# Optimization experiments

Hardware: AMD Instinct MI355X
Metric: run time of the kernel (lower is better)

Reference implementation:

```python
import jax, jax.numpy as jnp
import numpy as np

K_NBR = 64  # max_num_neighbors in radius()
M1, M2, M3 = 2048, 512, 512  # fps sample counts: 4096*0.5, 2048*0.25, 512*1.0
R1, R2, R3 = 0.2, 0.4, 1.0


def _fps_idx(pos, m):
    # Furthest point sampling, deterministic start at index 0. pos: [N,3] -> idx [m]
    d2 = jnp.sum((pos - pos[0]) ** 2, axis=-1)  # [N]

    def step(min_d2, _):
        nxt = jnp.argmax(min_d2).astype(jnp.int32)
        min_d2 = jnp.minimum(min_d2, jnp.sum((pos - pos[nxt]) ** 2, axis=-1))
        return min_d2, nxt

    _, rest = jax.lax.scan(step, d2, None, length=m - 1)
    return jnp.concatenate([jnp.zeros((1,), jnp.int32), rest])


def _ball_query(pos_src, pos_q, r, k):
    # Nearest up-to-k neighbors within radius r. Returns idx [M,k], valid mask [M,k].
    d2 = (jnp.sum(pos_q ** 2, -1)[:, None] + jnp.sum(pos_src ** 2, -1)[None, :]
          - 2.0 * pos_q @ pos_src.T)  # [M,N]
    neg = jnp.where(d2 <= r * r, -d2, -jnp.inf)
    vals, idx = jax.lax.top_k(neg, k)
    return idx, vals > -jnp.inf


def _sa_layer(x, pos, m, r, w1, b1, w2, b2):
    # x: [B,N,C], pos: [B,N,3] -> (x_new [B,m,Cout], pos_new [B,m,3])
    idx = jax.vmap(lambda p: _fps_idx(p, m))(pos)                     # [B,m]
    pos_q = jnp.take_along_axis(pos, idx[..., None], axis=1)         # [B,m,3]
    nbr, mask = jax.vmap(lambda s, q: _ball_query(s, q, r, K_NBR))(pos, pos_q)
    gather = jax.vmap(lambda a, i: a[i])                              # [N,C],[m,k]->[m,k,C]
    x_j = gather(x, nbr)                                              # [B,m,k,C]
    pos_j = gather(pos, nbr)                                          # [B,m,k,3]
    # PointNetConv message: MLP(concat(x_j, pos_j - pos_i)), max-aggregate
    msg = jnp.concatenate([x_j, pos_j - pos_q[:, :, None, :]], axis=-1)
    h = jnp.maximum(msg @ w1 + b1, 0.0) @ w2 + b2                     # [B,m,k,Cout]
    h = jnp.where(mask[..., None], h, -jnp.inf)
    out = jnp.max(h, axis=2)
    out = jnp.where(jnp.any(mask, axis=2, keepdims=True), out, 0.0)   # empty -> 0
    return out, pos_q


def setup_inputs() -> dict:
    key = jax.random.key(0)
    ks = jax.random.split(key, 8)
    B, N, C3 = 8, 4096, 128
    pos = jax.random.uniform(ks[0], (B, N, 3), jnp.float32)
    batch = jnp.repeat(jnp.arange(B, dtype=jnp.int32)[:, None], N, axis=1)

    def lin(k, ci, co):
        kw, kb = jax.random.split(k)
        s = 1.0 / np.sqrt(ci)
        return (jax.random.uniform(kw, (ci, co), jnp.float32, -s, s),
                jax.random.uniform(kb, (co,), jnp.float32, -s, s))

    w11, b11 = lin(ks[1], 3 + 3, 32)
    w12, b12 = lin(ks[2], 32, 32)
    w21, b21 = lin(ks[3], 32 + 3, 64)
    w22, b22 = lin(ks[4], 64, 64)
    w31, b31 = lin(ks[5], 64 + 3, C3)
    w32, b32 = lin(ks[6], C3, C3)
    return dict(pos=pos, batch=batch,
                w11=w11, b11=b11, w12=w12, b12=b12,
                w21=w21, b21=b21, w22=w22, b22=b22,
                w31=w31, b31=b31, w32=w32, b32=b32)


def reference(pos, batch, w11, b11, w12, b12, w21, b21, w22, b22, w31, b31, w32, b32):
    # Layer 1 uses positions as features (x = pos in encoder forward)
    x1, p1 = _sa_layer(pos, pos, M1, R1, w11, b11, w12, b12)
    x2, p2 = _sa_layer(x1, p1, M2, R2, w21, b21, w22, b22)
    x3, p3 = _sa_layer(x2, p2, M3, R3, w31, b31, w32, b32)
    return x3, p3, batch[:, :M3]
```

## Files before the change

### kernel.cpp

```cpp
#include <hip/hip_runtime.h>
#include <hip/hip_bf16.h>
#include <float.h>

typedef unsigned long long u64;

static __device__ __forceinline__ float d2_rn(float ax, float ay, float az,
                                              float bx, float by, float bz) {
  float dx = __fsub_rn(ax, bx), dy = __fsub_rn(ay, by), dz = __fsub_rn(az, bz);
  return __fadd_rn(__fadd_rn(__fmul_rn(dx, dx), __fmul_rn(dy, dy)), __fmul_rn(dz, dz));
}

static __device__ __forceinline__ void merge2(u64& a1, u64& a2, u64 b1, u64 b2) {
  bool agt = a1 > b1;
  u64 m1 = agt ? a1 : b1;
  u64 lo = agt ? b1 : a1;
  u64 cs = agt ? a2 : b2;
  a1 = m1;
  a2 = lo > cs ? lo : cs;
}

static __device__ __forceinline__ u64 pack_key(float v, int i) {
  if (v < 0.f) return 0ull;
  return ((u64)__float_as_uint(v) << 32) | (unsigned)(~i);
}

template<int CTRL>
static __device__ __forceinline__ u64 dpp_u64(u64 x) {
  unsigned lo = (unsigned)__builtin_amdgcn_update_dpp(0, (int)(unsigned)x, CTRL, 0xF, 0xF, true);
  unsigned hi = (unsigned)__builtin_amdgcn_update_dpp(0, (int)(unsigned)(x >> 32), CTRL, 0xF, 0xF, true);
  return ((u64)hi << 32) | lo;
}

template<int CTRL>
static __device__ __forceinline__ void merge_dpp(u64& a1, u64& a2) {
  u64 b1 = dpp_u64<CTRL>(a1);
  u64 b2 = dpp_u64<CTRL>(a2);
  merge2(a1, a2, b1, b2);
}

static __device__ __forceinline__ void wave_top2_dpp(u64& a1, u64& a2) {
  merge_dpp<0xB1>(a1, a2);
  merge_dpp<0x4E>(a1, a2);
  merge_dpp<0x141>(a1, a2);
  merge_dpp<0x140>(a1, a2);
  merge_dpp<0x142>(a1, a2);
  merge_dpp<0x143>(a1, a2);
}

template<int N, int M, int NPT, int T>
static __device__ void fps_body(const float* __restrict__ P, float* __restrict__ O,
                                char* smem) {
  constexpr int W = T / 64;
  static_assert(N == T * NPT, "layout");
  float* xs = (float*)smem;
  float* ys = xs + N;
  float* zs = ys + N;
  uint4* slots = (uint4*)(zs + N);
  const int tid = threadIdx.x;
  const int lane = tid & 63, wv = tid >> 6;

  for (int j = tid; j < N; j += T) {
    xs[j] = P[3 * j]; ys[j] = P[3 * j + 1]; zs[j] = P[3 * j + 2];
  }
  __syncthreads();

  const float c0x = xs[0], c0y = ys[0], c0z = zs[0];
  if (tid == 0) { O[0] = c0x; O[1] = c0y; O[2] = c0z; }

  float md[NPT], px[NPT], py[NPT], pz[NPT];
  float v1 = -1.f, v2 = -1.f; int i1 = 0, i2 = 0;
  #pragma unroll
  for (int k = 0; k < NPT; ++k) {
    int j = tid + k * T;
    px[k] = xs[j]; py[k] = ys[j]; pz[k] = zs[j];
    float m = d2_rn(px[k], py[k], pz[k], c0x, c0y, c0z);
    md[k] = m;
    if (m > v2) { if (m > v1) { v2=v1; i2=i1; v1=m; i1=j; } else { v2=m; i2=j; } }
  }

  u64 a1 = pack_key(v1, i1), a2 = pack_key(v2, i2);
  wave_top2_dpp(a1, a2);
  if (lane == 63)
    slots[wv] = make_uint4((unsigned)a1, (unsigned)(a1 >> 32),
                           (unsigned)a2, (unsigned)(a2 >> 32));

  int t = 1, phase = 0;
  while (t < M) {
    __syncthreads();
    uint4 s = slots[phase * W + (lane & (W - 1))];
    a1 = ((u64)s.y << 32) | s.x;
    a2 = ((u64)s.w << 32) | s.z;
    merge_dpp<0xB1>(a1, a2);
    merge_dpp<0x4E>(a1, a2);
    merge_dpp<0x141>(a1, a2);

    const int j1 = (int)(~(unsigned)a1);
    const float c1x = xs[j1], c1y = ys[j1], c1z = zs[j1];
    const float v2f = __uint_as_float((unsigned)(a2 >> 32));

    bool hit = false;
    float c2x = 0.f, c2y = 0.f, c2z = 0.f;
    if (t + 1 < M && v2f > 0.f) {
      int j2 = (int)(~(unsigned)a2);
      c2x = xs[j2]; c2y = ys[j2]; c2z = zs[j2];
      float dd = d2_rn(c2x, c2y, c2z, c1x, c1y, c1z);
      hit = (dd >= v2f);
    }

    if (tid == 0) {
      O[3 * t] = c1x; O[3 * t + 1] = c1y; O[3 * t + 2] = c1z;
      if (hit) { O[3 * t + 3] = c2x; O[3 * t + 4] = c2y; O[3 * t + 5] = c2z; }
    }

    v1 = -1.f; v2 = -1.f; i1 = 0; i2 = 0;
    if (hit) {
      #pragma unroll
      for (int k = 0; k < NPT; ++k) {
        float m = md[k];
        m = fminf(m, d2_rn(px[k], py[k], pz[k], c1x, c1y, c1z));
        m = fminf(m, d2_rn(px[k], py[k], pz[k], c2x, c2y, c2z));
        md[k] = m;
        int j = tid + k * T;
        if (m > v2) { if (m > v1) { v2=v1; i2=i1; v1=m; i1=j; } else { v2=m; i2=j; } }
      }
    } else {
      #pragma unroll
      for (int k = 0; k < NPT; ++k) {
        float m = fminf(md[k], d2_rn(px[k], py[k], pz[k], c1x, c1y, c1z));
        md[k] = m;
        int j = tid + k * T;
        if (m > v2) { if (m > v1) { v2=v1; i2=i1; v1=m; i1=j; } else { v2=m; i2=j; } }
      }
    }

    a1 = pack_key(v1, i1); a2 = pack_key(v2, i2);
    wave_top2_dpp(a1, a2);
    if (lane == 63)
      slots[(phase ^ 1) * W + wv] = make_uint4((unsigned)a1, (unsigned)(a1 >> 32),
                                               (unsigned)a2, (unsigned)(a2 >> 32));
    phase ^= 1;
    t += hit ? 2 : 1;
  }
}

template<int N, int M, int NPT>
__global__ __launch_bounds__(512) void fps_kernel(const float* __restrict__ pos,
                                                  float* __restrict__ out) {
  __shared__ __align__(16) char smem[3 * N * 4 + 2 * 8 * 16];
  fps_body<N, M, NPT, 512>(pos + (size_t)blockIdx.x * N * 3,
                           out + (size_t)blockIdx.x * M * 3, smem);
}

template<int C, int H>
__global__ void g_kernel(const float* __restrict__ x, const float* __restrict__ pos,
                         const float* __restrict__ W, float* __restrict__ g, int rows) {
  int idx = blockIdx.x * 256 + threadIdx.x;
  if (idx >= rows * H) return;
  int row = idx / H, h = idx - row * H;
  const float* xr = x + (size_t)row * C;
  const float* pr = pos + (size_t)row * 3;
  float acc = 0.f;
  for (int c = 0; c < C; ++c) acc = fmaf(xr[c], W[c * H + h], acc);
  #pragma unroll
  for (int c = 0; c < 3; ++c) acc = fmaf(pr[c], W[(C + c) * H + h], acc);
  g[idx] = acc;
}

template<int N, int H, int C, int QB>
__global__ __launch_bounds__(256) void sa_kernel(
    const float* __restrict__ src,
    const float* __restrict__ g,
    const float* __restrict__ qpos,
    const float* __restrict__ W2,
    const float* __restrict__ b1v,
    const float* __restrict__ W1p,
    const float* __restrict__ b2v,
    float r2, int M,
    float* __restrict__ out)
{
  constexpr int TPS = C / 2;
  constexpr int SG  = 256 / TPS;
  constexpr int JT  = SG * 4;
  constexpr int STRIDE = JT + 4;
  const int tid = threadIdx.x;
  const int b = blockIdx.y;
  const int sgi = tid / TPS;
  const int c2 = 2 * (tid - sgi * TPS);

  __shared__ __align__(16) __hip_bfloat16 sW2h[H * C];
  __shared__ float sD2[N];
  __shared__ float sT[H];
  __shared__ __align__(16) float sHj[STRIDE * H];
  __shared__ float sScr[512];
  __shared__ int   sNbr[64];
  __shared__ int   sWS[4];
  __shared__ int   sCnt, sNn, sNc, sBin, sBefore;
  __shared__ float sTauV; __shared__ int sTauI;

  int*   sHist  = (int*)sScr;
  float* sCand  = sScr + 256;
  int*   sCandI = (int*)(sScr + 320);
  float* sRed   = sScr;

  const float* srcb = src + (size_t)b * N * 3;
  const float* gb   = g   + (size_t)b * N * H;

  for (int e = tid; e < H * C; e += 256) sW2h[e] = __float2bfloat16(W2[e]);

  for (int qi = 0; qi < QB; ++qi) {
    const int i = blockIdx.x * QB + qi;
    const float* qp = qpos + ((size_t)b * M + i) * 3;
    const float qx = qp[0], qy = qp[1], qz = qp[2];
    const float qq = __fadd_rn(__fadd_rn(__fmul_rn(qx, qx), __fmul_rn(qy, qy)),
                               __fmul_rn(qz, qz));
    if (tid < H)
      sT[tid] = fmaf(qx, W1p[tid], fmaf(qy, W1p[H + tid], fmaf(qz, W1p[2 * H + tid], -b1v[tid])));
    if (tid == 0) { sCnt = 0; sNn = 0; sNc = 0; }
    sHist[tid] = 0;
    __syncthreads();

    int lc = 0;
    for (int j = tid; j < N; j += 256) {
      float sx = srcb[3 * j], sy = srcb[3 * j + 1], sz = srcb[3 * j + 2];
      float ss  = __fadd_rn(__fadd_rn(__fmul_rn(sx, sx), __fmul_rn(sy, sy)), __fmul_rn(sz, sz));
      float dot = __fadd_rn(__fadd_rn(__fmul_rn(qx, sx), __fmul_rn(qy, sy)), __fmul_rn(qz, sz));
      float d2  = __fsub_rn(__fadd_rn(qq, ss), __fmul_rn(2.0f, dot));
      sD2[j] = d2;
      lc += (d2 <= r2) ? 1 : 0;
    }
    #pragma unroll
    for (int off = 32; off > 0; off >>= 1) lc += __shfl_xor(lc, off, 64);
    if ((tid & 63) == 0) atomicAdd(&sCnt, lc);
    __syncthreads();
    const int cnt = sCnt;

    float tauv; int taui;
    if (cnt <= 64) {
      tauv = r2; taui = 0x7fffffff;
    } else {
      const float scale = 256.0f / r2;
      for (int j = tid; j < N; j += 256) {
        float d2 = sD2[j];
        if (d2 <= r2) {
          int bin = (int)(d2 * scale);
          bin = bin < 0 ? 0 : (bin > 255 ? 255 : bin);
          atomicAdd(&sHist[bin], 1);
        }
      }
      __syncthreads();
      int cbin = sHist[tid];
      int lane = tid & 63, wvi = tid >> 6;
      int v = cbin;
      #pragma unroll
      for (int off = 1; off < 64; off <<= 1) {
        int o = __shfl_up(v, off, 64);
        if (lane >= off) v += o;
      }
      if (lane == 63) sWS[wvi] = v;
      __syncthreads();
      int wadd = 0;
      for (int w = 0; w < wvi; ++w) wadd += sWS[w];
      int incl = v + wadd, excl = incl - cbin;
      if (excl < 64 && incl >= 64) { sBin = tid; sBefore = excl; }
      __syncthreads();
      const int bstar = sBin;
      const int kneed = 64 - sBefore;
      for (int j = tid; j < N; j += 256) {
        float d2 = sD2[j];
        if (d2 <= r2) {
          int bin = (int)(d2 * scale);
          bin = bin < 0 ? 0 : (bin > 255 ? 255 : bin);
          if (bin == bstar) {
            int p = atomicAdd(&sNc, 1);
            if (p < 64) { sCand[p] = d2; sCandI[p] = j; }
          }
        }
      }
      __syncthreads();
      if (tid == 0) {
        int nc = sNc < 64 ? sNc : 64;
        for (int a = 1; a < nc; ++a) {
          float dv = sCand[a]; int di = sCandI[a];
          int p = a - 1;
          while (p >= 0 && (sCand[p] > dv || (sCand[p] == dv && sCandI[p] > di))) {
            sCand[p + 1] = sCand[p]; sCandI[p + 1] = sCandI[p]; --p;
          }
          sCand[p + 1] = dv; sCandI[p + 1] = di;
        }
        int kk = (kneed < nc ? kneed : nc) - 1; if (kk < 0) kk = 0;
        sTauV = sCand[kk]; sTauI = sCandI[kk];
      }
      __syncthreads();
      tauv = sTauV; taui = sTauI;
    }

    for (int j = tid; j < N; j += 256) {
      float d2 = sD2[j];
      if (d2 < tauv || (d2 == tauv && j <= taui)) {
        int p = atomicAdd(&sNn, 1);
        if (p < 64) sNbr[p] = j;
      }
    }
    __syncthreads();
    const int nn = sNn < 64 ? sNn : 64;

    float m0 = -FLT_MAX, m1 = -FLT_MAX;
    for (int t0 = 0; t0 < nn; t0 += JT) {
      int jt = nn - t0; if (jt > JT) jt = JT;
      __syncthreads();
      for (int e = tid; e < JT * H; e += 256) {
        int jj = e / H, h = e - jj * H;
        float hv = 0.f;
        if (jj < jt) {
          int j = sNbr[t0 + jj];
          hv = gb[(size_t)j * H + h] - sT[h];
          hv = hv > 0.f ? hv : 0.f;
        }
        sHj[h * STRIDE + jj] = hv;
      }
      __syncthreads();
      float a0 = 0, a1 = 0, a2 = 0, a3 = 0, c0 = 0, c1 = 0, c2a = 0, c3 = 0;
      const int jbase = sgi * 4;
      for (int h = 0; h < H; ++h) {
        float4 hv = *reinterpret_cast<const float4*>(&sHj[h * STRIDE + jbase]);
        __hip_bfloat162 wp = *reinterpret_cast<const __hip_bfloat162*>(&sW2h[h * C + c2]);
        float wx = __bfloat162float(wp.x), wy = __bfloat162float(wp.y);
        a0 = fmaf(hv.x, wx, a0); a1 = fmaf(hv.y, wx, a1);
        a2 = fmaf(hv.z, wx, a2); a3 = fmaf(hv.w, wx, a3);
        c0 = fmaf(hv.x, wy, c0); c1 = fmaf(hv.y, wy, c1);
        c2a = fmaf(hv.z, wy, c2a); c3 = fmaf(hv.w, wy, c3);
      }
      if (jbase + 0 < jt) { m0 = fmaxf(m0, a0); m1 = fmaxf(m1, c0); }
      if (jbase + 1 < jt) { m0 = fmaxf(m0, a1); m1 = fmaxf(m1, c1); }
      if (jbase + 2 < jt) { m0 = fmaxf(m0, a2); m1 = fmaxf(m1, c2a); }
      if (jbase + 3 < jt) { m0 = fmaxf(m0, a3); m1 = fmaxf(m1, c3); }
    }
    __syncthreads();
    sRed[sgi * C + c2]     = m0;
    sRed[sgi * C + c2 + 1] = m1;
    __syncthreads();
    if (tid < TPS) {
      int c = 2 * tid;
      float M0 = sRed[c], M1 = sRed[c + 1];
      #pragma unroll
      for (int s2 = 1; s2 < SG; ++s2) {
        M0 = fmaxf(M0, sRed[s2 * C + c]);
        M1 = fmaxf(M1, sRed[s2 * C + c + 1]);
      }
      float o0 = nn > 0 ? M0 + b2v[c]     : 0.f;
      float o1 = nn > 0 ? M1 + b2v[c + 1] : 0.f;
      float* orow = out + (((size_t)b * M) + i) * C;
      orow[c] = o0; orow[c + 1] = o1;
    }
    __syncthreads();
  }
}

__global__ void tail_kernel(const float* __restrict__ p3, float* __restrict__ d_out) {
  int i = blockIdx.x * 256 + threadIdx.x;
  if (i < 8 * 512 * 3) d_out[524288 + i] = p3[i];
  if (i < 8 * 512)     d_out[536576 + i] = (float)(i >> 9);
}

extern "C" void kernel_launch(void* const* d_in, const int* in_sizes, int n_in,
                              void* d_out, int out_size, void* d_ws, size_t ws_size,
                              hipStream_t stream) {
  (void)in_sizes; (void)n_in; (void)out_size; (void)ws_size;
  const float* pos = (const float*)d_in[0];
  const float* w11 = (const float*)d_in[2];
  const float* b11 = (const float*)d_in[3];
  const float* w12 = (const float*)d_in[4];
  const float* b12 = (const float*)d_in[5];
  const float* w21 = (const float*)d_in[6];
  const float* b21 = (const float*)d_in[7];
  const float* w22 = (const float*)d_in[8];
  const float* b22 = (const float*)d_in[9];
  const float* w31 = (const float*)d_in[10];
  const float* b31 = (const float*)d_in[11];
  const float* w32 = (const float*)d_in[12];
  const float* b32 = (const float*)d_in[13];

  float* ws = (float*)d_ws;
  float* p1 = ws; ws += 8 * 2048 * 3;
  float* p2 = ws; ws += 8 * 512 * 3;
  float* p3 = ws; ws += 8 * 512 * 3;
  float* g1 = ws; ws += 8 * 4096 * 32;
  float* x1 = ws; ws += 8 * 2048 * 32;
  float* g2 = ws; ws += 8 * 2048 * 64;
  float* x2 = ws; ws += 8 * 512 * 64;
  float* g3 = ws; ws += 8 * 512 * 128;
  float* x3 = (float*)d_out;

  fps_kernel<4096, 2048, 8><<<dim3(8), dim3(512), 0, stream>>>(pos, p1);
  g_kernel<3, 32><<<dim3(8 * 4096 * 32 / 256), dim3(256), 0, stream>>>(pos, pos, w11, g1, 8 * 4096);
  sa_kernel<4096, 32, 32, 8><<<dim3(2048 / 8, 8), dim3(256), 0, stream>>>(
      pos, g1, p1, w12, b11, w11 + 3 * 32, b12, 0.04f, 2048, x1);
  fps_kernel<2048, 512, 4><<<dim3(8), dim3(512), 0, stream>>>(p1, p2);
  g_kernel<32, 64><<<dim3(8 * 2048 * 64 / 256), dim3(256), 0, stream>>>(x1, p1, w21, g2, 8 * 2048);
  sa_kernel<2048, 64, 64, 8><<<dim3(512 / 8, 8), dim3(256), 0, stream>>>(
      p1, g2, p2, w22, b21, w21 + 32 * 64, b22, 0.16f, 512, x2);
  fps_kernel<512, 512, 1><<<dim3(8), dim3(512), 0, stream>>>(p2, p3);
  g_kernel<64, 128><<<dim3(8 * 512 * 128 / 256), dim3(256), 0, stream>>>(x2, p2, w31, g3, 8 * 512);
  sa_kernel<512, 128, 128, 8><<<dim3(64, 8), dim3(256), 0, stream>>>(
      p2, g3, p3, w32, b31, w31 + 64 * 128, b32, 1.0f, 512, x3);
  tail_kernel<<<dim3(48), dim3(256), 0, stream>>>(p3, (float*)d_out);
}
```

Baseline: 2.431 ms.

## Speculatively accept up to four FPS centers per iteration from per-wave top-2 pool

The furthest-point-sampling loop now gathers the per-wave top-2 candidates into a pool and greedily accepts up to four successive centers per barrier round. A candidate is accepted only if its distance to every already-accepted center is at least its key value, so it matches what sequential FPS would pick. The block size drops from 512 to 256 threads, with twice the points per thread, so the pool fits within eight lanes. The aim is to cut the number of serialized sync/reduce iterations, at the cost of more distance work per point per round and fewer threads per block.

```diff
diff --git a/kernel.cpp b/kernel.cpp
--- a/kernel.cpp
+++ b/kernel.cpp
@@ -47,10 +47,29 @@
   merge_dpp<0x143>(a1, a2);
 }
 
+static __device__ __forceinline__ u64 max8_dpp(u64 k) {
+  u64 o = dpp_u64<0xB1>(k);  if (o > k) k = o;
+  o = dpp_u64<0x4E>(k);      if (o > k) k = o;
+  o = dpp_u64<0x141>(k);     if (o > k) k = o;
+  return k;
+}
+
+#define FPS_UPDATE(PP)                                                                 \
+  { _Pragma("unroll")                                                                  \
+    for (int k = 0; k < NPT; ++k) {                                                    \
+      float m = md[k];                                                                 \
+      _Pragma("unroll")                                                                \
+      for (int mm = 0; mm < (PP); ++mm)                                                \
+        m = fminf(m, d2_rn(px[k], py[k], pz[k], ax[mm], ay[mm], az[mm]));              \
+      md[k] = m; int j = tid + k * T;                                                  \
+      if (m > v2) { if (m > v1) { v2=v1; i2=i1; v1=m; i1=j; } else { v2=m; i2=j; } }   \
+    } }
+
 template<int N, int M, int NPT, int T>
 static __device__ void fps_body(const float* __restrict__ P, float* __restrict__ O,
                                 char* smem) {
   constexpr int W = T / 64;
+  constexpr int POOL = 2 * W;
   static_assert(N == T * NPT, "layout");
   float* xs = (float*)smem;
   float* ys = xs + N;
@@ -87,50 +106,61 @@
   int t = 1, phase = 0;
   while (t < M) {
     __syncthreads();
-    uint4 s = slots[phase * W + (lane & (W - 1))];
-    a1 = ((u64)s.y << 32) | s.x;
-    a2 = ((u64)s.w << 32) | s.z;
-    merge_dpp<0xB1>(a1, a2);
-    merge_dpp<0x4E>(a1, a2);
-    merge_dpp<0x141>(a1, a2);
-
-    const int j1 = (int)(~(unsigned)a1);
-    const float c1x = xs[j1], c1y = ys[j1], c1z = zs[j1];
-    const float v2f = __uint_as_float((unsigned)(a2 >> 32));
-
-    bool hit = false;
-    float c2x = 0.f, c2y = 0.f, c2z = 0.f;
-    if (t + 1 < M && v2f > 0.f) {
-      int j2 = (int)(~(unsigned)a2);
-      c2x = xs[j2]; c2y = ys[j2]; c2z = zs[j2];
-      float dd = d2_rn(c2x, c2y, c2z, c1x, c1y, c1z);
-      hit = (dd >= v2f);
-    }
-
+    u64 key = 0;
+    float kx = 0.f, ky = 0.f, kz = 0.f;
+    if (lane < POOL) {
+      uint4 s = slots[phase * W + (lane >> 1)];
+      key = (lane & 1) ? (((u64)s.w << 32) | s.z) : (((u64)s.y << 32) | s.x);
+      int idx = (int)(~(unsigned)key);
+      kx = xs[idx]; ky = ys[idx]; kz = zs[idx];
+    }
+    float ax[4], ay[4], az[4];
+    int p = 0;
+    {
+      unsigned usedWaves = 0;
+      const int room = (M - t) < 4 ? (M - t) : 4;
+      bool stop = false;
+      #pragma unroll
+      for (int e = 0; e < 4; ++e) {
+        if (!stop && p < room) {
+          u64 g = max8_dpp(key);
+          u64 ball = __ballot(lane < POOL && key != 0 && key == g);
+          if (ball == 0) { stop = true; }
+          else {
+            int s = __ffsll(ball) - 1;
+            float vk = __uint_as_float((unsigned)__builtin_amdgcn_readlane((int)(unsigned)(key >> 32), s));
+            float cx = __int_as_float(__builtin_amdgcn_readlane(__float_as_int(kx), s));
+            float cy = __int_as_float(__builtin_amdgcn_readlane(__float_as_int(ky), s));
+            float cz = __int_as_float(__builtin_amdgcn_readlane(__float_as_int(kz), s));
+            bool ok = true;
+            #pragma unroll
+            for (int mm = 0; mm < 3; ++mm)
+              if (mm < p) ok = ok && (d2_rn(cx, cy, cz, ax[mm], ay[mm], az[mm]) >= vk);
+            if (!ok) { stop = true; }
+            else {
+              ax[p] = cx; ay[p] = cy; az[p] = cz; ++p;
+              if (lane == s) key = 0;
+              unsigned wbit = 1u << (s >> 1);
+              if (usedWaves & wbit) stop = true;
+              usedWaves |= wbit;
+            }
+          }
+        }
+      }
+    }
     if (tid == 0) {
-      O[3 * t] = c1x; O[3 * t + 1] = c1y; O[3 * t + 2] = c1z;
-      if (hit) { O[3 * t + 3] = c2x; O[3 * t + 4] = c2y; O[3 * t + 5] = c2z; }
-    }
-
+      #pragma unroll
+      for (int mm = 0; mm < 4; ++mm)
+        if (mm < p) {
+          O[3 * (t + mm)] = ax[mm]; O[3 * (t + mm) + 1] = ay[mm]; O[3 * (t + mm) + 2] = az[mm];
+        }
+    }
     v1 = -1.f; v2 = -1.f; i1 = 0; i2 = 0;
-    if (hit) {
-      #pragma unroll
-      for (int k = 0; k < NPT; ++k) {
-        float m = md[k];
-        m = fminf(m, d2_rn(px[k], py[k], pz[k], c1x, c1y, c1z));
-        m = fminf(m, d2_rn(px[k], py[k], pz[k], c2x, c2y, c2z));
-        md[k] = m;
-        int j = tid + k * T;
-        if (m > v2) { if (m > v1) { v2=v1; i2=i1; v1=m; i1=j; } else { v2=m; i2=j; } }
-      }
-    } else {
-      #pragma unroll
-      for (int k = 0; k < NPT; ++k) {
-        float m = fminf(md[k], d2_rn(px[k], py[k], pz[k], c1x, c1y, c1z));
-        md[k] = m;
-        int j = tid + k * T;
-        if (m > v2) { if (m > v1) { v2=v1; i2=i1; v1=m; i1=j; } else { v2=m; i2=j; } }
-      }
+    switch (p) {
+      case 1:  FPS_UPDATE(1); break;
+      case 2:  FPS_UPDATE(2); break;
+      case 3:  FPS_UPDATE(3); break;
+      default: FPS_UPDATE(4); break;
     }
 
     a1 = pack_key(v1, i1); a2 = pack_key(v2, i2);
@@ -139,15 +169,15 @@
       slots[(phase ^ 1) * W + wv] = make_uint4((unsigned)a1, (unsigned)(a1 >> 32),
                                                (unsigned)a2, (unsigned)(a2 >> 32));
     phase ^= 1;
-    t += hit ? 2 : 1;
+    t += p;
   }
 }
 
 template<int N, int M, int NPT>
-__global__ __launch_bounds__(512) void fps_kernel(const float* __restrict__ pos,
+__global__ __launch_bounds__(256) void fps_kernel(const float* __restrict__ pos,
                                                   float* __restrict__ out) {
-  __shared__ __align__(16) char smem[3 * N * 4 + 2 * 8 * 16];
-  fps_body<N, M, NPT, 512>(pos + (size_t)blockIdx.x * N * 3,
+  __shared__ __align__(16) char smem[3 * N * 4 + 2 * 4 * 16];
+  fps_body<N, M, NPT, 256>(pos + (size_t)blockIdx.x * N * 3,
                            out + (size_t)blockIdx.x * M * 3, smem);
 }
 
@@ -391,15 +421,15 @@
   float* g3 = ws; ws += 8 * 512 * 128;
   float* x3 = (float*)d_out;
 
-  fps_kernel<4096, 2048, 8><<<dim3(8), dim3(512), 0, stream>>>(pos, p1);
+  fps_kernel<4096, 2048, 16><<<dim3(8), dim3(256), 0, stream>>>(pos, p1);
   g_kernel<3, 32><<<dim3(8 * 4096 * 32 / 256), dim3(256), 0, stream>>>(pos, pos, w11, g1, 8 * 4096);
   sa_kernel<4096, 32, 32, 8><<<dim3(2048 / 8, 8), dim3(256), 0, stream>>>(
       pos, g1, p1, w12, b11, w11 + 3 * 32, b12, 0.04f, 2048, x1);
-  fps_kernel<2048, 512, 4><<<dim3(8), dim3(512), 0, stream>>>(p1, p2);
+  fps_kernel<2048, 512, 8><<<dim3(8), dim3(256), 0, stream>>>(p1, p2);
   g_kernel<32, 64><<<dim3(8 * 2048 * 64 / 256), dim3(256), 0, stream>>>(x1, p1, w21, g2, 8 * 2048);
   sa_kernel<2048, 64, 64, 8><<<dim3(512 / 8, 8), dim3(256), 0, stream>>>(
       p1, g2, p2, w22, b21, w21 + 32 * 64, b22, 0.16f, 512, x2);
-  fps_kernel<512, 512, 1><<<dim3(8), dim3(512), 0, stream>>>(p2, p3);
+  fps_kernel<512, 512, 2><<<dim3(8), dim3(256), 0, stream>>>(p2, p3);
   g_kernel<64, 128><<<dim3(8 * 512 * 128 / 256), dim3(256), 0, stream>>>(x2, p2, w31, g3, 8 * 512);
   sa_kernel<512, 128, 128, 8><<<dim3(64, 8), dim3(256), 0, stream>>>(
       p2, g3, p3, w32, b31, w31 + 64 * 128, b32, 1.0f, 512, x3);
```

After: 3.057 ms. 1.26x slower.
